# Kernel tuning notes

Measured on AMD Instinct MI355X. Metric: run time of the kernel, lower is better.

The kernel has to match this reference:

```python
import jax, jax.numpy as jnp
import numpy as np

SEQ, H, NC = 20, 128, 100000

def _lstm_cell(x, h, c, Wih, Whh, bih, bhh):
    # gates: [B, 4H] in PyTorch order i, f, g, o
    g = x @ Wih.T + bih + h @ Whh.T + bhh
    i, f, gg, o = jnp.split(g, 4, axis=-1)
    c2 = jax.nn.sigmoid(f) * c + jax.nn.sigmoid(i) * jnp.tanh(gg)
    h2 = jax.nn.sigmoid(o) * jnp.tanh(c2)
    return h2, c2

def setup_inputs() -> dict:
    key = jax.random.key(0)
    ks = jax.random.split(key, 24)
    u = lambda k, shp, bound: jax.random.uniform(k, shp, jnp.float32, -bound, bound)
    s1 = 1.0 / np.sqrt(H)       # PyTorch LSTMCell init bound, hidden_size=H
    s2 = 1.0 / np.sqrt(2 * H)   # combined cell, hidden_size=2H
    kn = lambda k, shp: jax.random.normal(k, shp, jnp.float32) * np.sqrt(2.0 / shp[1])  # kaiming_normal_
    return {
        'x': jax.random.normal(ks[0], (SEQ, 1, H), jnp.float32),
        'h0f': kn(ks[1], (1, H)), 'c0f': kn(ks[2], (1, H)),
        'h0b': kn(ks[3], (1, H)), 'c0b': kn(ks[4], (1, H)),
        'h0l': kn(ks[5], (1, 2 * H)), 'c0l': kn(ks[6], (1, 2 * H)),
        'Wih_f': u(ks[7], (4 * H, H), s1), 'Whh_f': u(ks[8], (4 * H, H), s1),
        'bih_f': u(ks[9], (4 * H,), s1), 'bhh_f': u(ks[10], (4 * H,), s1),
        'Wih_b': u(ks[11], (4 * H, H), s1), 'Whh_b': u(ks[12], (4 * H, H), s1),
        'bih_b': u(ks[13], (4 * H,), s1), 'bhh_b': u(ks[14], (4 * H,), s1),
        'Wih_l': u(ks[15], (8 * H, 2 * H), s2), 'Whh_l': u(ks[16], (8 * H, 2 * H), s2),
        'bih_l': u(ks[17], (8 * H,), s2), 'bhh_l': u(ks[18], (8 * H,), s2),
        'Wlin': u(ks[19], (NC, 2 * H), 1.0 / np.sqrt(2 * H)),
        'blin': u(ks[20], (NC,), 1.0 / np.sqrt(2 * H)),
    }

def reference(x, h0f, c0f, h0b, c0b, h0l, c0l,
              Wih_f, Whh_f, bih_f, bhh_f,
              Wih_b, Whh_b, bih_b, bhh_b,
              Wih_l, Whh_l, bih_l, bhh_l,
              Wlin, blin):
    xs = x.reshape(SEQ, 1, H)

    def step_f(carry, xt):
        h, c = _lstm_cell(xt, carry[0], carry[1], Wih_f, Whh_f, bih_f, bhh_f)
        return (h, c), h
    _, fwd = jax.lax.scan(step_f, (h0f, c0f), xs)          # [SEQ, 1, H]

    def step_b(carry, xt):
        h, c = _lstm_cell(xt, carry[0], carry[1], Wih_b, Whh_b, bih_b, bhh_b)
        return (h, c), h
    # backward list is kept in reversed-scan order (NOT flipped back), per source zip
    _, bwd = jax.lax.scan(step_b, (h0b, c0b), xs[::-1])    # [SEQ, 1, H]

    comb = jnp.concatenate([fwd, bwd], axis=-1)            # [SEQ, 1, 2H]

    def step_l(carry, xt):
        h, c = _lstm_cell(xt, carry[0], carry[1], Wih_l, Whh_l, bih_l, bhh_l)
        return (h, c), h
    _, hl = jax.lax.scan(step_l, (h0l, c0l), comb)         # [SEQ, 1, 2H]

    fb = hl.reshape(SEQ, 2 * H)
    return fb @ Wlin.T + blin                              # [SEQ, NC]
```

## Files before the change

kernel.cpp:

```cpp
#include <hip/hip_runtime.h>
#include <stdint.h>

#define SEQ  20
#define H1   128
#define H2   256
#define NCLS 100000

#define AQ  __ATOMIC_ACQUIRE
#define RL  __ATOMIC_RELEASE
#define RX  __ATOMIC_RELAXED
#define AG  __HIP_MEMORY_SCOPE_AGENT

#define KEEPF4(v) asm volatile("" : "+v"((v).x), "+v"((v).y), "+v"((v).z), "+v"((v).w))

__device__ __forceinline__ float sigm(float x) { return 1.0f / (1.0f + __expf(-x)); }
__device__ __forceinline__ float tanhfast(float x) {
    float e = __expf(-2.0f * fabsf(x));
    float t = (1.0f - e) / (1.0f + e);
    return copysignf(t, x);
}

__global__ __launch_bounds__(1024, 1) void k_lstm(
    const float* __restrict__ x,
    const float* __restrict__ h0f, const float* __restrict__ c0f,
    const float* __restrict__ h0b, const float* __restrict__ c0b,
    const float* __restrict__ WihF, const float* __restrict__ WhhF,
    const float* __restrict__ bihF, const float* __restrict__ bhhF,
    const float* __restrict__ WihB, const float* __restrict__ WhhB,
    const float* __restrict__ bihB, const float* __restrict__ bhhB,
    const float* __restrict__ Wihl, const float* __restrict__ Whhl,
    const float* __restrict__ bihl, const float* __restrict__ bhhl,
    const float* __restrict__ h0l,  const float* __restrict__ c0l,
    float* __restrict__ comb,
    float* __restrict__ fb,
    float* __restrict__ hg2,
    int* __restrict__ flags)
{
    __shared__ __align__(16) float smem[16032];
    const int bid = blockIdx.x;
    if (bid & 7) return;
    const int role = bid >> 3;
    const int tid  = threadIdx.x;

    if (role < 2) {
        const int dir = role;
        const float* Wih = dir ? WihB : WihF;
        const float* Whh = dir ? WhhB : WhhF;
        const float* bih = dir ? bihB : bihF;
        const float* bhh = dir ? bhhB : bhhF;
        const float* h0  = dir ? h0b  : h0f;
        const float* c0  = dir ? c0b  : c0f;

        float* xs      = smem;
        float* hcur    = xs + 2560;
        float* biasL   = hcur + 128;
        float* gxs     = biasL + 512;
        float* partial = gxs + 10752;

        for (int i = tid; i < SEQ * H1; i += 1024) xs[i] = x[i];
        if (tid < 4 * H1) biasL[tid] = bih[tid] + bhh[tid];
        if (tid < H1) hcur[tid] = h0[tid];
        float cregA = 0.f, cregB = 0.f;
        if (tid < 64) { cregA = c0[tid]; cregB = c0[tid + 64]; }

        const int pr = tid >> 1, ph = tid & 1;
        {
            float4 wf[16];
            const float4* p = (const float4*)(Wih + pr * H1 + ph * 64);
#pragma unroll
            for (int j = 0; j < 16; ++j) { wf[j] = p[j]; KEEPF4(wf[j]); }
            __syncthreads();
            for (int t = 0; t < SEQ; ++t) {
                const int tx = dir ? (SEQ - 1 - t) : t;
                const float4* xp = (const float4*)(xs + tx * H1 + ph * 64);
                float a = 0.f;
#pragma unroll
                for (int j = 0; j < 16; ++j) {
                    float4 v = xp[j];
                    a += wf[j].x * v.x + wf[j].y * v.y + wf[j].z * v.z + wf[j].w * v.w;
                }
                a += __shfl_xor(a, 1);
                if (ph == 0) gxs[pr * 21 + t] = a + biasL[pr];
            }
        }

        const int cg = tid >> 8, r0 = (tid & 255) * 2;
        float4 wa[8], wb[8];
        {
            const float4* pa = (const float4*)(Whh + r0 * H1 + cg * 32);
            const float4* pb = (const float4*)(Whh + (r0 + 1) * H1 + cg * 32);
#pragma unroll
            for (int j = 0; j < 8; ++j) {
                wa[j] = pa[j]; KEEPF4(wa[j]);
                wb[j] = pb[j]; KEEPF4(wb[j]);
            }
        }
        __syncthreads();

        for (int t = 0; t < SEQ; ++t) {
            const float4* hp = (const float4*)(hcur + cg * 32);
            float a0 = 0.f, a1 = 0.f;
#pragma unroll
            for (int j = 0; j < 8; ++j) {
                float4 v = hp[j];
                a0 += wa[j].x * v.x + wa[j].y * v.y + wa[j].z * v.z + wa[j].w * v.w;
                a1 += wb[j].x * v.x + wb[j].y * v.y + wb[j].z * v.z + wb[j].w * v.w;
            }
            *(float2*)(partial + cg * 520 + r0) = make_float2(a0, a1);
            __syncthreads();
            if (tid < 64) {
                const int c = tid;
                float s0[4], s1[4];
#pragma unroll
                for (int g = 0; g < 4; ++g) {
                    float accA = gxs[(g * H1 + c) * 21 + t];
                    float accB = gxs[(g * H1 + c + 64) * 21 + t];
#pragma unroll
                    for (int q = 0; q < 4; ++q) {
                        accA += partial[q * 520 + g * H1 + c];
                        accB += partial[q * 520 + g * H1 + c + 64];
                    }
                    s0[g] = accA; s1[g] = accB;
                }
                float cnA = sigm(s0[1]) * cregA + sigm(s0[0]) * tanhfast(s0[2]);
                float cnB = sigm(s1[1]) * cregB + sigm(s1[0]) * tanhfast(s1[2]);
                cregA = cnA; cregB = cnB;
                float hA = sigm(s0[3]) * tanhfast(cnA);
                float hB = sigm(s1[3]) * tanhfast(cnB);
                hcur[c] = hA; hcur[c + 64] = hB;
                __hip_atomic_store(&comb[t * H2 + dir * H1 + c],      hA, RX, AG);
                __hip_atomic_store(&comb[t * H2 + dir * H1 + c + 64], hB, RX, AG);
                if (tid == 0)
                    __hip_atomic_store(&flags[dir * 32], t + 1, RL, AG);
            }
            __syncthreads();
        }
    } else {
        const int s = role - 2;
        float* ct    = smem;
        float* hc2   = ct + 256;
        float* bias2 = hc2 + 256;
        float* part2 = bias2 + 128;

        const int cg = tid >> 7;
        const int L  = tid & 127;
        const int R  = (L >> 5) * H2 + s * 32 + (L & 31);

        float4 wih[8], whh[8];
        {
            const float4* pi = (const float4*)(Wihl + (size_t)R * H2 + cg * 32);
            const float4* pw = (const float4*)(Whhl + (size_t)R * H2 + cg * 32);
#pragma unroll
            for (int j = 0; j < 8; ++j) {
                wih[j] = pi[j]; KEEPF4(wih[j]);
                whh[j] = pw[j]; KEEPF4(whh[j]);
            }
        }
        if (tid < 128) bias2[tid] = bihl[R] + bhhl[R];
        if (tid < H2)  hc2[tid] = h0l[tid];
        float creg = (tid < 32) ? c0l[s * 32 + tid] : 0.0f;

        if (tid >= 512 && tid < 576) {
            const int l = tid - 512;
            const int f = (l < 32) ? 0 : 32;
            while (__hip_atomic_load(&flags[f], AQ, AG) < 1)
                __builtin_amdgcn_s_sleep(1);
#pragma unroll
            for (int j = 0; j < 4; ++j)
                ct[l * 4 + j] = __hip_atomic_load(&comb[l * 4 + j], RX, AG);
        }
        __syncthreads();

        for (int t = 0; t < SEQ; ++t) {
            {
                const float4* cp = (const float4*)(ct  + cg * 32);
                const float4* hp = (const float4*)(hc2 + cg * 32);
                float a = 0.f;
#pragma unroll
                for (int j = 0; j < 8; ++j) {
                    float4 cv = cp[j], hv = hp[j];
                    a += wih[j].x * cv.x + wih[j].y * cv.y
                       + wih[j].z * cv.z + wih[j].w * cv.w
                       + whh[j].x * hv.x + whh[j].y * hv.y
                       + whh[j].z * hv.z + whh[j].w * hv.w;
                }
                part2[cg * 132 + L] = a;
            }
            __syncthreads();
            if (tid < 32) {
                float sg[4];
#pragma unroll
                for (int g = 0; g < 4; ++g) {
                    float acc = bias2[g * 32 + tid];
#pragma unroll
                    for (int q = 0; q < 8; ++q)
                        acc += part2[q * 132 + g * 32 + tid];
                    sg[g] = acc;
                }
                float cn = sigm(sg[1]) * creg + sigm(sg[0]) * tanhfast(sg[2]);
                creg = cn;
                float hn = sigm(sg[3]) * tanhfast(cn);
                hc2[s * 32 + tid] = hn;
                __hip_atomic_store(&fb[t * H2 + s * 32 + tid], hn, RX, AG);
                __hip_atomic_store(&hg2[(t & 1) * H2 + s * 32 + tid], hn, RX, AG);
                if (tid == 0)
                    __hip_atomic_store(&flags[(2 + s) * 32], t + 1, RL, AG);
            } else if (tid >= 64 && tid < 128 && t + 1 < SEQ) {
                const int l  = tid - 64;
                const int sh = l >> 3;
                if (sh != s) {
                    while (__hip_atomic_load(&flags[(2 + sh) * 32], AQ, AG) < t + 1)
                        __builtin_amdgcn_s_sleep(1);
                    const int base = sh * 32 + (l & 7) * 4;
#pragma unroll
                    for (int j = 0; j < 4; ++j)
                        hc2[base + j] =
                            __hip_atomic_load(&hg2[(t & 1) * H2 + base + j], RX, AG);
                }
            } else if (tid >= 512 && tid < 576 && t + 1 < SEQ) {
                const int l = tid - 512;
                const int f = (l < 32) ? 0 : 32;
                while (__hip_atomic_load(&flags[f], AQ, AG) < t + 2)
                    __builtin_amdgcn_s_sleep(1);
#pragma unroll
                for (int j = 0; j < 4; ++j)
                    ct[l * 4 + j] =
                        __hip_atomic_load(&comb[(t + 1) * H2 + l * 4 + j], RX, AG);
            }
            __syncthreads();
        }
    }
}

__global__ __launch_bounds__(256, 4) void k_out_v(
    const float* __restrict__ Wlin, const float* __restrict__ blin,
    const float* __restrict__ fb, float* __restrict__ out)
{
    __shared__ float fbs[H2][SEQ];
    const int tid = threadIdx.x;
    for (int t = 0; t < SEQ; ++t) fbs[tid][t] = fb[t * H2 + tid];
    __syncthreads();

    int n = blockIdx.x * 256 + tid;
    if (n >= NCLS) return;
    float acc[SEQ];
    float bv = blin[n];
#pragma unroll
    for (int t = 0; t < SEQ; ++t) acc[t] = bv;

    const float* wp = Wlin + (size_t)n * H2;
    for (int k = 0; k < H2; k += 4) {
        float4 wv = *(const float4*)(wp + k);
#pragma unroll
        for (int t = 0; t < SEQ; t += 4) {
            float4 f0 = *(const float4*)(&fbs[k][t]);
            float4 f1 = *(const float4*)(&fbs[k + 1][t]);
            float4 f2 = *(const float4*)(&fbs[k + 2][t]);
            float4 f3 = *(const float4*)(&fbs[k + 3][t]);
            acc[t]     += wv.x * f0.x + wv.y * f1.x + wv.z * f2.x + wv.w * f3.x;
            acc[t + 1] += wv.x * f0.y + wv.y * f1.y + wv.z * f2.y + wv.w * f3.y;
            acc[t + 2] += wv.x * f0.z + wv.y * f1.z + wv.z * f2.z + wv.w * f3.z;
            acc[t + 3] += wv.x * f0.w + wv.y * f1.w + wv.z * f2.w + wv.w * f3.w;
        }
    }
#pragma unroll
    for (int t = 0; t < SEQ; ++t)
        out[(size_t)t * NCLS + n] = acc[t];
}

extern "C" void kernel_launch(void* const* d_in, const int* in_sizes, int n_in,
                              void* d_out, int out_size, void* d_ws, size_t ws_size,
                              hipStream_t stream)
{
    const float* x    = (const float*)d_in[0];
    const float* h0f_ = (const float*)d_in[1];
    const float* c0f_ = (const float*)d_in[2];
    const float* h0b_ = (const float*)d_in[3];
    const float* c0b_ = (const float*)d_in[4];
    const float* h0l_ = (const float*)d_in[5];
    const float* c0l_ = (const float*)d_in[6];
    const float* WihF = (const float*)d_in[7];
    const float* WhhF = (const float*)d_in[8];
    const float* bihF = (const float*)d_in[9];
    const float* bhhF = (const float*)d_in[10];
    const float* WihB = (const float*)d_in[11];
    const float* WhhB = (const float*)d_in[12];
    const float* bihB = (const float*)d_in[13];
    const float* bhhB = (const float*)d_in[14];
    const float* Wihl = (const float*)d_in[15];
    const float* Whhl = (const float*)d_in[16];
    const float* bihl = (const float*)d_in[17];
    const float* bhhl = (const float*)d_in[18];
    const float* Wlin = (const float*)d_in[19];
    const float* blin = (const float*)d_in[20];

    char* ws = (char*)d_ws;
    int*   flags = (int*)ws;
    float* hg2   = (float*)(ws + 2048);
    float* comb  = (float*)(ws + 4096);
    float* fb    = (float*)(ws + 24576);

    hipMemsetAsync(flags, 0, 2048, stream);

    k_lstm<<<80, 1024, 0, stream>>>(
        x, h0f_, c0f_, h0b_, c0b_,
        WihF, WhhF, bihF, bhhF,
        WihB, WhhB, bihB, bhhB,
        Wihl, Whhl, bihl, bhhl,
        h0l_, c0l_,
        comb, fb, hg2, flags);
    k_out_v<<<391, 256, 0, stream>>>(Wlin, blin, fb, (float*)d_out);
}
```

Baseline: 372.6 us.

## Split output projection rows across four lanes with shuffle reduction and staged stores

The output projection kernel now assigns 4 threads to each class row. Each thread handles an interleaved quarter of the 256-wide dot product, so the 4 lanes together read a contiguous 64-byte chunk of the weight row, and the next chunk is prefetched while the current one is used. Partial sums are combined with xor shuffles, staged in a padded shared buffer, then written to the output with coalesced stores that add the bias. The grid grows to 64 classes per block, giving about four times as many blocks to fill the GPU. The shared layout uses a row stride of 21 floats to avoid bank conflicts, which leaves the float4 LDS reads unaligned. That is a correctness and performance risk.

```diff
diff --git a/kernel.cpp b/kernel.cpp
--- a/kernel.cpp
+++ b/kernel.cpp
@@ -232,40 +232,78 @@
     }
 }
 
-__global__ __launch_bounds__(256, 4) void k_out_v(
+__global__ __launch_bounds__(256, 4) void k_out_p(
     const float* __restrict__ Wlin, const float* __restrict__ blin,
     const float* __restrict__ fb, float* __restrict__ out)
 {
-    __shared__ float fbs[H2][SEQ];
+    __shared__ float fbs[H2 * 21];
+    __shared__ float obuf[64 * 21];
     const int tid = threadIdx.x;
-    for (int t = 0; t < SEQ; ++t) fbs[tid][t] = fb[t * H2 + tid];
+    const int c   = tid >> 2;
+    const int q   = tid & 3;
+    const int n   = blockIdx.x * 64 + c;
+
+    for (int t = 0; t < SEQ; ++t) fbs[tid * 21 + t] = fb[t * H2 + tid];
     __syncthreads();
 
-    int n = blockIdx.x * 256 + tid;
-    if (n >= NCLS) return;
     float acc[SEQ];
-    float bv = blin[n];
-#pragma unroll
-    for (int t = 0; t < SEQ; ++t) acc[t] = bv;
-
-    const float* wp = Wlin + (size_t)n * H2;
-    for (int k = 0; k < H2; k += 4) {
-        float4 wv = *(const float4*)(wp + k);
-#pragma unroll
-        for (int t = 0; t < SEQ; t += 4) {
-            float4 f0 = *(const float4*)(&fbs[k][t]);
-            float4 f1 = *(const float4*)(&fbs[k + 1][t]);
-            float4 f2 = *(const float4*)(&fbs[k + 2][t]);
-            float4 f3 = *(const float4*)(&fbs[k + 3][t]);
-            acc[t]     += wv.x * f0.x + wv.y * f1.x + wv.z * f2.x + wv.w * f3.x;
-            acc[t + 1] += wv.x * f0.y + wv.y * f1.y + wv.z * f2.y + wv.w * f3.y;
-            acc[t + 2] += wv.x * f0.z + wv.y * f1.z + wv.z * f2.z + wv.w * f3.z;
-            acc[t + 3] += wv.x * f0.w + wv.y * f1.w + wv.z * f2.w + wv.w * f3.w;
-        }
-    }
-#pragma unroll
-    for (int t = 0; t < SEQ; ++t)
-        out[(size_t)t * NCLS + n] = acc[t];
+#pragma unroll
+    for (int t = 0; t < SEQ; ++t) acc[t] = 0.f;
+
+    if (n < NCLS) {
+        const float* wrow = Wlin + (size_t)n * H2;
+        float4 wv = *(const float4*)(wrow + q * 4);
+#pragma unroll 1
+        for (int j = 0; j < 15; ++j) {
+            float4 wnext = *(const float4*)(wrow + (j + 1) * 16 + q * 4);
+            const float* f0 = fbs + (j * 16 + q * 4) * 21;
+#pragma unroll
+            for (int t = 0; t < SEQ; t += 4) {
+                float4 a0 = *(const float4*)(f0 + t);
+                float4 a1 = *(const float4*)(f0 + 21 + t);
+                float4 a2 = *(const float4*)(f0 + 42 + t);
+                float4 a3 = *(const float4*)(f0 + 63 + t);
+                acc[t]     += wv.x * a0.x + wv.y * a1.x + wv.z * a2.x + wv.w * a3.x;
+                acc[t + 1] += wv.x * a0.y + wv.y * a1.y + wv.z * a2.y + wv.w * a3.y;
+                acc[t + 2] += wv.x * a0.z + wv.y * a1.z + wv.z * a2.z + wv.w * a3.z;
+                acc[t + 3] += wv.x * a0.w + wv.y * a1.w + wv.z * a2.w + wv.w * a3.w;
+            }
+            wv = wnext;
+        }
+        {
+            const float* f0 = fbs + (240 + q * 4) * 21;
+#pragma unroll
+            for (int t = 0; t < SEQ; t += 4) {
+                float4 a0 = *(const float4*)(f0 + t);
+                float4 a1 = *(const float4*)(f0 + 21 + t);
+                float4 a2 = *(const float4*)(f0 + 42 + t);
+                float4 a3 = *(const float4*)(f0 + 63 + t);
+                acc[t]     += wv.x * a0.x + wv.y * a1.x + wv.z * a2.x + wv.w * a3.x;
+                acc[t + 1] += wv.x * a0.y + wv.y * a1.y + wv.z * a2.y + wv.w * a3.y;
+                acc[t + 2] += wv.x * a0.z + wv.y * a1.z + wv.z * a2.z + wv.w * a3.z;
+                acc[t + 3] += wv.x * a0.w + wv.y * a1.w + wv.z * a2.w + wv.w * a3.w;
+            }
+        }
+    }
+
+#pragma unroll
+    for (int t = 0; t < SEQ; ++t) {
+        acc[t] += __shfl_xor(acc[t], 1);
+        acc[t] += __shfl_xor(acc[t], 2);
+    }
+    if (q == 0) {
+#pragma unroll
+        for (int t = 0; t < SEQ; ++t) obuf[c * 21 + t] = acc[t];
+    }
+    __syncthreads();
+
+    const int base = blockIdx.x * 64;
+    for (int i = tid; i < 64 * SEQ; i += 256) {
+        const int t = i >> 6, cc = i & 63;
+        const int n2 = base + cc;
+        if (n2 < NCLS)
+            out[(size_t)t * NCLS + n2] = obuf[cc * 21 + t] + blin[n2];
+    }
 }
 
 extern "C" void kernel_launch(void* const* d_in, const int* in_sizes, int n_in,
@@ -309,5 +347,5 @@
         Wihl, Whhl, bihl, bhhl,
         h0l_, c0l_,
         comb, fb, hg2, flags);
-    k_out_v<<<391, 256, 0, stream>>>(Wlin, blin, fb, (float*)d_out);
+    k_out_p<<<(NCLS + 63) / 64, 256, 0, stream>>>(Wlin, blin, fb, (float*)d_out);
 }
```

Measured after the change: 506.8 us. 36.0% more time.
